# Kernel tuning notes

Hardware: AMD Instinct MI355X
Metric: run time of the kernel (lower is better)

## Reference

```python
import jax, jax.numpy as jnp
import numpy as np

N_NODES = 100000
N_EDGES = 600000
HID = 128
N_ETYPES = 8


def setup_inputs() -> dict:
    key = jax.random.key(0)
    ks = jax.random.split(key, 10)
    s = 1.0 / np.sqrt(HID)
    return {
        "h": jax.random.normal(ks[0], (N_NODES, HID), dtype=jnp.float32),
        "edge_index": jax.random.randint(ks[1], (2, N_EDGES), 0, N_NODES, dtype=jnp.int64),
        "edge_type": jax.random.randint(ks[2], (N_EDGES,), 0, N_ETYPES, dtype=jnp.int64),
        # per-edge-type Linear(hidden, hidden): weight (T, H_out, H_in) stored as (T, H_in, H_out) for einsum
        "message_W": jax.random.uniform(ks[3], (N_ETYPES, HID, HID), jnp.float32, -s, s),
        "message_b": jax.random.uniform(ks[4], (N_ETYPES, HID), jnp.float32, -s, s),
        # GRUCell params (torch layout): w_ih (3H, H), w_hh (3H, H), b_ih (3H,), b_hh (3H,)
        "gru_w_ih": jax.random.uniform(ks[5], (3 * HID, HID), jnp.float32, -s, s),
        "gru_w_hh": jax.random.uniform(ks[6], (3 * HID, HID), jnp.float32, -s, s),
        "gru_b_ih": jax.random.uniform(ks[7], (3 * HID,), jnp.float32, -s, s),
        "gru_b_hh": jax.random.uniform(ks[8], (3 * HID,), jnp.float32, -s, s),
    }


def reference(h, edge_index, edge_type, message_W, message_b,
              gru_w_ih, gru_w_hh, gru_b_ih, gru_b_hh):
    num_nodes = h.shape[0]
    src, dst = edge_index[0], edge_index[1]

    # Transform every node by every edge-type Linear once: (N, T, H).
    # Equivalent to per-type msg = h[src] @ W[t].T + b[t] gathered by edge type.
    all_msgs = jnp.einsum('nh,thd->ntd', h, message_W) + message_b  # (N, T, H)
    msg = all_msgs[src, edge_type]                                   # (E, H) gather
    messages = jax.ops.segment_sum(msg, dst, num_segments=num_nodes)  # scatter-add

    # GRUCell: r,z,n gates (torch semantics)
    gi = messages @ gru_w_ih.T + gru_b_ih  # (N, 3H)
    gh = h @ gru_w_hh.T + gru_b_hh         # (N, 3H)
    i_r, i_z, i_n = jnp.split(gi, 3, axis=-1)
    h_r, h_z, h_n = jnp.split(gh, 3, axis=-1)
    r = jax.nn.sigmoid(i_r + h_r)
    z = jax.nn.sigmoid(i_z + h_z)
    n = jnp.tanh(i_n + r * h_n)
    return (1.0 - z) * n + z * h
```

## Files before the change

### kernel.cpp

```cpp
#include <hip/hip_runtime.h>

#define HID 128
#define NTY 8

typedef __attribute__((ext_vector_type(8))) short bf16x8;
typedef __attribute__((ext_vector_type(4))) float f32x4;

__device__ __forceinline__ unsigned short f2bf(float x) {
    unsigned u = __float_as_uint(x);
    u += 0x7FFF + ((u >> 16) & 1);
    return (unsigned short)(u >> 16);
}
__device__ __forceinline__ float bf2f(unsigned short s) {
    return __uint_as_float(((unsigned)s) << 16);
}
__device__ __forceinline__ float sigmoidf_fast(float x) {
    return 1.f / (1.f + __expf(-x));
}
__device__ __forceinline__ float tanhf_fast(float x) {
    return 1.f - 2.f / (1.f + __expf(2.f * x));
}

__global__ void conv_h_kernel(const float* __restrict__ h, unsigned short* __restrict__ hbf, int n) {
    int i = blockIdx.x * 256 + threadIdx.x;
    if (i < n) hbf[i] = f2bf(h[i]);
}
__global__ void conv_W_kernel(const float* __restrict__ W, unsigned short* __restrict__ WbfT) {
    int i = blockIdx.x * 256 + threadIdx.x;
    int t = i >> 14, rem = i & 16383, d = rem >> 7, k = rem & 127;
    WbfT[(t << 14) + (d << 7) + k] = f2bf(W[(t << 14) + (k << 7) + d]);
}
__global__ void conv_wpk_kernel(const float* __restrict__ wih, const float* __restrict__ whh,
                                unsigned short* __restrict__ wpk) {
    int i = blockIdx.x * 256 + threadIdx.x;
    if (i >= 8 * 3 * 128 * 32) return;
    int kk = i & 31;
    int rest = i >> 5;
    int d = rest & 127;
    int rest2 = rest >> 7;
    int g3 = rest2 % 3, kc = rest2 / 3;
    float v;
    if (kc < 4) v = wih[(g3 * 128 + d) * 128 + kc * 32 + kk];
    else        v = whh[(g3 * 128 + d) * 128 + (kc - 4) * 32 + kk];
    wpk[i] = f2bf(v);
}

__global__ void hist_kernel(const int* __restrict__ etype, const int* __restrict__ ei,
                            int E, int* __restrict__ tcnt, int* __restrict__ deg) {
    __shared__ int lc[NTY];
    if (threadIdx.x < NTY) lc[threadIdx.x] = 0;
    __syncthreads();
    int stride = gridDim.x * blockDim.x;
    for (int i = blockIdx.x * blockDim.x + threadIdx.x; i < E; i += stride) {
        atomicAdd(&lc[etype[i]], 1);
        if (deg) atomicAdd(&deg[ei[E + i]], 1);
    }
    __syncthreads();
    if (threadIdx.x < NTY) atomicAdd(&tcnt[threadIdx.x], lc[threadIdx.x]);
}

__global__ void scan_type_kernel(const int* __restrict__ tcnt, int* __restrict__ tcur) {
    if (threadIdx.x == 0) {
        int off = 0;
        for (int t = 0; t < NTY; ++t) { tcur[t] = off; off += (tcnt[t] + 127) & ~127; }
    }
}

__global__ void scanA_kernel(const int* __restrict__ deg, int* __restrict__ start,
                             int* __restrict__ bsum, int N) {
    __shared__ int s[256];
    int i = blockIdx.x * 256 + threadIdx.x;
    int v = (i < N) ? deg[i] : 0;
    s[threadIdx.x] = v;
    __syncthreads();
    for (int off = 1; off < 256; off <<= 1) {
        int t = (threadIdx.x >= off) ? s[threadIdx.x - off] : 0;
        __syncthreads();
        s[threadIdx.x] += t;
        __syncthreads();
    }
    if (i < N) start[i] = s[threadIdx.x] - v;
    if (threadIdx.x == 255) bsum[blockIdx.x] = s[255];
}

__global__ void scanB_kernel(int* __restrict__ bsum, int nb) {
    __shared__ int s[512];
    int tx = threadIdx.x;
    int v = (tx < nb) ? bsum[tx] : 0;
    s[tx] = v;
    __syncthreads();
    for (int off = 1; off < 512; off <<= 1) {
        int t = (tx >= off) ? s[tx - off] : 0;
        __syncthreads();
        s[tx] += t;
        __syncthreads();
    }
    if (tx < nb) bsum[tx] = s[tx] - v;
}

__global__ void scanC_kernel(int* __restrict__ start, const int* __restrict__ bsum,
                             int* __restrict__ dcur, int N, int E) {
    int i = blockIdx.x * 256 + threadIdx.x;
    if (i < N) {
        int v = start[i] + bsum[blockIdx.x];
        start[i] = v;
        dcur[i] = v;
    }
    if (i == 0) start[N] = E;
}

__global__ __launch_bounds__(256) void scatter_agg(
    const int* __restrict__ etype, const int* __restrict__ ei, int E,
    int* __restrict__ tcur, int* __restrict__ dcur,
    int* __restrict__ sortedT, int* __restrict__ q, int mode)
{
    __shared__ int lcnt[NTY];
    __shared__ int lbase[NTY];
    int tx = threadIdx.x;
    int chunk = (E + gridDim.x - 1) / gridDim.x;
    int s = blockIdx.x * chunk;
    int e = s + chunk; if (e > E) e = E;
    if (tx < NTY) lcnt[tx] = 0;
    __syncthreads();
    for (int i = s + tx; i < e; i += 256)
        atomicAdd(&lcnt[etype[i]], 1);
    __syncthreads();
    if (tx < NTY) {
        lbase[tx] = atomicAdd(&tcur[tx], lcnt[tx]);
        lcnt[tx] = 0;
    }
    __syncthreads();
    for (int i = s + tx; i < e; i += 256) {
        int t = etype[i];
        int lp = atomicAdd(&lcnt[t], 1);
        sortedT[lbase[t] + lp] = i;
        if (mode) q[i] = atomicAdd(&dcur[ei[E + i]], 1);
    }
}

__global__ __launch_bounds__(256) void msg_gemm(
    const unsigned short* __restrict__ hbf, const int* __restrict__ ei, int E,
    const int* __restrict__ etype, const unsigned short* __restrict__ WbfT,
    const float* __restrict__ bias, const int* __restrict__ sortedT,
    const int* __restrict__ q, unsigned short* __restrict__ M,
    float* __restrict__ msum, int mode)
{
    __shared__ unsigned short hs[128][136];
    __shared__ unsigned short Bs[128][40];
    __shared__ int srcs[128], aux[128];
    __shared__ int stype;

    int tx = threadIdx.x;
    int base = blockIdx.x * 128;
    if (tx < 128) {
        int id = sortedT[base + tx];
        srcs[tx] = (id >= 0) ? ei[id] : -1;
        aux[tx]  = (id >= 0) ? (mode ? ei[E + id] : q[id]) : -1;
    }
    if (tx == 0) { int id0 = sortedT[base]; stype = (id0 >= 0) ? etype[id0] : -1; }
    __syncthreads();
    int t = stype;
    if (t < 0) return;

    const unsigned short* Wb = WbfT + (t << 14);

    for (int f = tx; f < 2048; f += 256) {
        int row = f >> 4, c8 = (f & 15) * 8;
        int s = srcs[row]; if (s < 0) s = 0;
        *(uint4*)&hs[row][c8] = *(const uint4*)&hbf[(size_t)s * 128 + c8];
    }

    int lane = tx & 63, w = tx >> 6;
    int r0 = (w >> 1) * 64, c0 = (w & 1) * 64;
    int lr = lane & 15, quad = lane >> 4;
    f32x4 acc[4][4] = {};

    for (int kc = 0; kc < 4; ++kc) {
        __syncthreads();
        for (int f = tx; f < 512; f += 256) {
            int d = f >> 2, c8 = (f & 3) * 8;
            *(uint4*)&Bs[d][c8] = *(const uint4*)&Wb[(d << 7) + kc * 32 + c8];
        }
        __syncthreads();
        bf16x8 af[4], bfr[4];
        #pragma unroll
        for (int rb = 0; rb < 4; ++rb) af[rb]  = *(const bf16x8*)&hs[r0 + rb * 16 + lr][kc * 32 + quad * 8];
        #pragma unroll
        for (int cb = 0; cb < 4; ++cb) bfr[cb] = *(const bf16x8*)&Bs[c0 + cb * 16 + lr][quad * 8];
        #pragma unroll
        for (int rb = 0; rb < 4; ++rb)
            #pragma unroll
            for (int cb = 0; cb < 4; ++cb)
                acc[rb][cb] = __builtin_amdgcn_mfma_f32_16x16x32_bf16(bfr[cb], af[rb], acc[rb][cb], 0, 0, 0);
    }

    float4 bv4[4];
    #pragma unroll
    for (int cb = 0; cb < 4; ++cb)
        bv4[cb] = *(const float4*)&bias[t * 128 + c0 + cb * 16 + quad * 4];

    #pragma unroll
    for (int rb = 0; rb < 4; ++rb) {
        int e = r0 + rb * 16 + lr;
        int mr = aux[e];
        if (mr < 0) continue;
        #pragma unroll
        for (int cb = 0; cb < 4; ++cb) {
            int d0 = c0 + cb * 16 + quad * 4;
            f32x4 a = acc[rb][cb];
            if (mode) {
                atomicAdd(&msum[(size_t)mr * 128 + d0 + 0], a[0] + bv4[cb].x);
                atomicAdd(&msum[(size_t)mr * 128 + d0 + 1], a[1] + bv4[cb].y);
                atomicAdd(&msum[(size_t)mr * 128 + d0 + 2], a[2] + bv4[cb].z);
                atomicAdd(&msum[(size_t)mr * 128 + d0 + 3], a[3] + bv4[cb].w);
            } else {
                uint2 v;
                v.x = (unsigned)f2bf(a[0] + bv4[cb].x) | ((unsigned)f2bf(a[1] + bv4[cb].y) << 16);
                v.y = (unsigned)f2bf(a[2] + bv4[cb].z) | ((unsigned)f2bf(a[3] + bv4[cb].w) << 16);
                *(uint2*)&M[(size_t)mr * 128 + d0] = v;
            }
        }
    }
}

__global__ __launch_bounds__(256) void gru_fused(
    const unsigned short* __restrict__ M, const int* __restrict__ start,
    const float* __restrict__ msum_fb, const unsigned short* __restrict__ hbf,
    const unsigned short* __restrict__ wpk, const float* __restrict__ bih,
    const float* __restrict__ bhh, const float* __restrict__ hf,
    float* __restrict__ out, int N, int mode)
{
    __shared__ unsigned short As[64][264];

    int tx = threadIdx.x;
    int n0 = blockIdx.x * 64;

    {
        int node = tx >> 2, qd = tx & 3;
        int n = n0 + node;
        int nc = (n < N) ? n : N - 1;
        float a[32];
        #pragma unroll
        for (int j = 0; j < 32; ++j) a[j] = 0.f;
        if (mode == 0) {
            int s = start[nc], e = start[nc + 1];
            for (int r = s; r < e; ++r) {
                #pragma unroll
                for (int j = 0; j < 4; ++j) {
                    uint4 v = *(const uint4*)&M[(size_t)r * 128 + qd * 32 + j * 8];
                    const unsigned short* pv = (const unsigned short*)&v;
                    #pragma unroll
                    for (int u = 0; u < 8; ++u) a[j * 8 + u] += bf2f(pv[u]);
                }
            }
        } else {
            #pragma unroll
            for (int j = 0; j < 8; ++j) {
                float4 v = *(const float4*)&msum_fb[(size_t)nc * 128 + qd * 32 + j * 4];
                a[j * 4 + 0] = v.x; a[j * 4 + 1] = v.y; a[j * 4 + 2] = v.z; a[j * 4 + 3] = v.w;
            }
        }
        unsigned short tmp[32];
        #pragma unroll
        for (int j = 0; j < 32; ++j) tmp[j] = f2bf(a[j]);
        #pragma unroll
        for (int j = 0; j < 4; ++j)
            *(uint4*)&As[node][qd * 32 + j * 8] = *(const uint4*)&tmp[j * 8];
        #pragma unroll
        for (int j = 0; j < 4; ++j)
            *(uint4*)&As[node][128 + qd * 32 + j * 8] =
                *(const uint4*)&hbf[(size_t)nc * 128 + qd * 32 + j * 8];
    }
    __syncthreads();

    int lane = tx & 63, w = tx >> 6;
    int rt = w & 1, cg = w >> 1;
    int lr = lane & 15, quad = lane >> 4;

    f32x4 aR[4][2] = {}, aZ[4][2] = {}, aI[4][2] = {}, aH[4][2] = {};

    #pragma unroll
    for (int kc = 0; kc < 4; ++kc) {
        bf16x8 af[2];
        #pragma unroll
        for (int r2 = 0; r2 < 2; ++r2)
            af[r2] = *(const bf16x8*)&As[rt * 32 + r2 * 16 + lr][kc * 32 + quad * 8];
        #pragma unroll
        for (int g3 = 0; g3 < 3; ++g3) {
            #pragma unroll
            for (int ct = 0; ct < 4; ++ct) {
                bf16x8 bf = *(const bf16x8*)&wpk[((size_t)((kc * 3 + g3) * 128) + cg * 64 + ct * 16 + lr) * 32 + quad * 8];
                #pragma unroll
                for (int r2 = 0; r2 < 2; ++r2) {
                    if (g3 == 0) aR[ct][r2] = __builtin_amdgcn_mfma_f32_16x16x32_bf16(bf, af[r2], aR[ct][r2], 0, 0, 0);
                    else if (g3 == 1) aZ[ct][r2] = __builtin_amdgcn_mfma_f32_16x16x32_bf16(bf, af[r2], aZ[ct][r2], 0, 0, 0);
                    else aI[ct][r2] = __builtin_amdgcn_mfma_f32_16x16x32_bf16(bf, af[r2], aI[ct][r2], 0, 0, 0);
                }
            }
        }
    }
    #pragma unroll
    for (int kc = 4; kc < 8; ++kc) {
        bf16x8 af[2];
        #pragma unroll
        for (int r2 = 0; r2 < 2; ++r2)
            af[r2] = *(const bf16x8*)&As[rt * 32 + r2 * 16 + lr][kc * 32 + quad * 8];
        #pragma unroll
        for (int g3 = 0; g3 < 3; ++g3) {
            #pragma unroll
            for (int ct = 0; ct < 4; ++ct) {
                bf16x8 bf = *(const bf16x8*)&wpk[((size_t)((kc * 3 + g3) * 128) + cg * 64 + ct * 16 + lr) * 32 + quad * 8];
                #pragma unroll
                for (int r2 = 0; r2 < 2; ++r2) {
                    if (g3 == 0) aR[ct][r2] = __builtin_amdgcn_mfma_f32_16x16x32_bf16(bf, af[r2], aR[ct][r2], 0, 0, 0);
                    else if (g3 == 1) aZ[ct][r2] = __builtin_amdgcn_mfma_f32_16x16x32_bf16(bf, af[r2], aZ[ct][r2], 0, 0, 0);
                    else aH[ct][r2] = __builtin_amdgcn_mfma_f32_16x16x32_bf16(bf, af[r2], aH[ct][r2], 0, 0, 0);
                }
            }
        }
    }

    #pragma unroll
    for (int ct = 0; ct < 4; ++ct) {
        int d0 = cg * 64 + ct * 16 + quad * 4;
        f32x4 bi_r = *(const f32x4*)&bih[d0];
        f32x4 bh_r = *(const f32x4*)&bhh[d0];
        f32x4 bi_z = *(const f32x4*)&bih[128 + d0];
        f32x4 bh_z = *(const f32x4*)&bhh[128 + d0];
        f32x4 bi_n = *(const f32x4*)&bih[256 + d0];
        f32x4 bh_n = *(const f32x4*)&bhh[256 + d0];
        #pragma unroll
        for (int r2 = 0; r2 < 2; ++r2) {
            int n = n0 + rt * 32 + r2 * 16 + lr;
            if (n >= N) continue;
            f32x4 h0 = *(const f32x4*)&hf[(size_t)n * 128 + d0];
            f32x4 o;
            #pragma unroll
            for (int j = 0; j < 4; ++j) {
                float r  = sigmoidf_fast(aR[ct][r2][j] + bi_r[j] + bh_r[j]);
                float z  = sigmoidf_fast(aZ[ct][r2][j] + bi_z[j] + bh_z[j]);
                float nn = tanhf_fast(aI[ct][r2][j] + bi_n[j] + r * (aH[ct][r2][j] + bh_n[j]));
                o[j] = (1.f - z) * nn + z * h0[j];
            }
            *(f32x4*)&out[(size_t)n * 128 + d0] = o;
        }
    }
}

extern "C" void kernel_launch(void* const* d_in, const int* in_sizes, int n_in,
                              void* d_out, int out_size, void* d_ws, size_t ws_size,
                              hipStream_t stream)
{
    const float* h     = (const float*)d_in[0];
    const int*   ei    = (const int*)d_in[1];
    const int*   etype = (const int*)d_in[2];
    const float* W     = (const float*)d_in[3];
    const float* b     = (const float*)d_in[4];
    const float* wih   = (const float*)d_in[5];
    const float* whh   = (const float*)d_in[6];
    const float* bih   = (const float*)d_in[7];
    const float* bhh   = (const float*)d_in[8];
    float* out = (float*)d_out;

    int E = in_sizes[1] / 2;
    int N = in_sizes[0] / HID;
    int capE = ((E + 127) / 128 + NTY) * 128;

    char* p = (char*)d_ws;
    auto alloc = [&](size_t bytes) { char* r = p; p += (bytes + 255) & ~(size_t)255; return r; };
    unsigned short* hbf  = (unsigned short*)alloc((size_t)N * 128 * 2);
    unsigned short* WbfT = (unsigned short*)alloc((size_t)8 * 128 * 128 * 2);
    unsigned short* wpk  = (unsigned short*)alloc((size_t)8 * 3 * 128 * 32 * 2);
    int* tcnt    = (int*)alloc(NTY * 4);
    int* tcur    = (int*)alloc(NTY * 4);
    int* sortedT = (int*)alloc((size_t)capE * 4);
    unsigned short* M = (unsigned short*)alloc((size_t)E * 128 * 2);
    int* q     = (int*)alloc((size_t)E * 4);
    int* deg   = (int*)alloc((size_t)N * 4);
    int* start = (int*)alloc((size_t)(N + 1) * 4);
    int* dcur  = (int*)alloc((size_t)N * 4);
    int* bsum  = (int*)alloc(512 * 4);
    int mode = ((size_t)(p - (char*)d_ws) <= ws_size) ? 0 : 1;

    hipMemsetAsync(tcnt, 0, NTY * 4, stream);
    hipMemsetAsync(sortedT, 0xFF, (size_t)capE * 4, stream);
    if (mode == 0) hipMemsetAsync(deg, 0, (size_t)N * 4, stream);
    else           hipMemsetAsync(out, 0, (size_t)N * 128 * 4, stream);

    conv_h_kernel<<<(N * 128 + 255) / 256, 256, 0, stream>>>(h, hbf, N * 128);
    conv_W_kernel<<<(8 * 128 * 128) / 256, 256, 0, stream>>>(W, WbfT);
    conv_wpk_kernel<<<(8 * 3 * 128 * 32 + 255) / 256, 256, 0, stream>>>(wih, whh, wpk);

    hist_kernel<<<1024, 256, 0, stream>>>(etype, ei, E, tcnt, (mode == 0) ? deg : nullptr);
    scan_type_kernel<<<1, 64, 0, stream>>>(tcnt, tcur);
    if (mode == 0) {
        int nbA = (N + 255) / 256;
        scanA_kernel<<<nbA, 256, 0, stream>>>(deg, start, bsum, N);
        scanB_kernel<<<1, 512, 0, stream>>>(bsum, nbA);
        scanC_kernel<<<nbA, 256, 0, stream>>>(start, bsum, dcur, N, E);
    }
    scatter_agg<<<256, 256, 0, stream>>>(etype, ei, E, tcur, dcur, sortedT, q, (mode == 0) ? 1 : 0);

    msg_gemm<<<capE / 128, 256, 0, stream>>>(hbf, ei, E, etype, WbfT, b, sortedT, q, M, out, mode);
    gru_fused<<<(N + 63) / 64, 256, 0, stream>>>(M, start, out, hbf, wpk, bih, bhh, h, out, N, mode);
}
```

Baseline: 411.7 us.

## Aggregate source features per (dst,type) before transform and fuse into GRU kernel

Edges are now sorted by (destination, edge type) with an 8-way counting sort. For each node and type, the bf16 source features are summed first and multiplied by W[t] afterwards, with the bias scaled by the edge count. The per-edge message GEMM and the E×128 intermediate buffer are gone, and the aggregation, the type GEMMs and the GRU all run in one kernel with weights pre-packed into MFMA fragment order. In exchange the gather loops are per-lane and serial, their length depends on node degree, and each node block repeats 8 small GEMMs.

```diff
diff --git a/kernel.cpp b/kernel.cpp
--- a/kernel.cpp
+++ b/kernel.cpp
@@ -2,6 +2,7 @@
 
 #define HID 128
 #define NTY 8
+#define SCAP 768
 
 typedef __attribute__((ext_vector_type(8))) short bf16x8;
 typedef __attribute__((ext_vector_type(4))) float f32x4;
@@ -25,45 +26,41 @@
     int i = blockIdx.x * 256 + threadIdx.x;
     if (i < n) hbf[i] = f2bf(h[i]);
 }
-__global__ void conv_W_kernel(const float* __restrict__ W, unsigned short* __restrict__ WbfT) {
-    int i = blockIdx.x * 256 + threadIdx.x;
-    int t = i >> 14, rem = i & 16383, d = rem >> 7, k = rem & 127;
-    WbfT[(t << 14) + (d << 7) + k] = f2bf(W[(t << 14) + (k << 7) + d]);
-}
-__global__ void conv_wpk_kernel(const float* __restrict__ wih, const float* __restrict__ whh,
-                                unsigned short* __restrict__ wpk) {
-    int i = blockIdx.x * 256 + threadIdx.x;
-    if (i >= 8 * 3 * 128 * 32) return;
-    int kk = i & 31;
-    int rest = i >> 5;
-    int d = rest & 127;
-    int rest2 = rest >> 7;
-    int g3 = rest2 % 3, kc = rest2 / 3;
+
+__global__ void conv_Wfrag_kernel(const float* __restrict__ W, unsigned short* __restrict__ wfr) {
+    int i = blockIdx.x * 256 + threadIdx.x;
+    int e = i & 7, f = (i >> 3) & 31, lane = (i >> 8) & 63, t = i >> 14;
+    int cb = f >> 2, kc = f & 3;
+    int lr = lane & 15, quad = lane >> 4;
+    int d = cb * 16 + lr;
+    int k = kc * 32 + quad * 8 + e;
+    wfr[i] = f2bf(W[(t << 14) + (k << 7) + d]);
+}
+
+__global__ void conv_wpkf_kernel(const float* __restrict__ wih, const float* __restrict__ whh,
+                                 unsigned short* __restrict__ wpkf) {
+    int i = blockIdx.x * 256 + threadIdx.x;
+    int e = i & 7;
+    int rest = i >> 3;
+    int lane = rest / 192;
+    int f = rest - lane * 192;
+    int kc = f / 24;
+    int f2 = f - kc * 24;
+    int g3 = f2 >> 3, ct = f2 & 7;
+    int lr = lane & 15, quad = lane >> 4;
+    int d = ct * 16 + lr;
+    int kk = quad * 8 + e;
     float v;
     if (kc < 4) v = wih[(g3 * 128 + d) * 128 + kc * 32 + kk];
     else        v = whh[(g3 * 128 + d) * 128 + (kc - 4) * 32 + kk];
-    wpk[i] = f2bf(v);
-}
-
-__global__ void hist_kernel(const int* __restrict__ etype, const int* __restrict__ ei,
-                            int E, int* __restrict__ tcnt, int* __restrict__ deg) {
-    __shared__ int lc[NTY];
-    if (threadIdx.x < NTY) lc[threadIdx.x] = 0;
-    __syncthreads();
+    wpkf[i] = f2bf(v);
+}
+
+__global__ void hist8_kernel(const int* __restrict__ etype, const int* __restrict__ ei,
+                             int E, int* __restrict__ deg8) {
     int stride = gridDim.x * blockDim.x;
-    for (int i = blockIdx.x * blockDim.x + threadIdx.x; i < E; i += stride) {
-        atomicAdd(&lc[etype[i]], 1);
-        if (deg) atomicAdd(&deg[ei[E + i]], 1);
-    }
-    __syncthreads();
-    if (threadIdx.x < NTY) atomicAdd(&tcnt[threadIdx.x], lc[threadIdx.x]);
-}
-
-__global__ void scan_type_kernel(const int* __restrict__ tcnt, int* __restrict__ tcur) {
-    if (threadIdx.x == 0) {
-        int off = 0;
-        for (int t = 0; t < NTY; ++t) { tcur[t] = off; off += (tcnt[t] + 127) & ~127; }
-    }
+    for (int i = blockIdx.x * blockDim.x + threadIdx.x; i < E; i += stride)
+        atomicAdd(&deg8[ei[E + i] * 8 + etype[i]], 1);
 }
 
 __global__ void scanA_kernel(const int* __restrict__ deg, int* __restrict__ start,
@@ -83,266 +80,216 @@
     if (threadIdx.x == 255) bsum[blockIdx.x] = s[255];
 }
 
-__global__ void scanB_kernel(int* __restrict__ bsum, int nb) {
-    __shared__ int s[512];
+__global__ void scanBbig_kernel(int* __restrict__ bsum, int nb) {
+    __shared__ int s[256];
     int tx = threadIdx.x;
-    int v = (tx < nb) ? bsum[tx] : 0;
-    s[tx] = v;
+    int C = (nb + 255) / 256;
+    int lo = tx * C, hi = lo + C; if (hi > nb) hi = nb;
+    int sum = 0;
+    for (int j = lo; j < hi; ++j) sum += bsum[j];
+    s[tx] = sum;
     __syncthreads();
-    for (int off = 1; off < 512; off <<= 1) {
+    for (int off = 1; off < 256; off <<= 1) {
         int t = (tx >= off) ? s[tx - off] : 0;
         __syncthreads();
         s[tx] += t;
         __syncthreads();
     }
-    if (tx < nb) bsum[tx] = s[tx] - v;
-}
-
-__global__ void scanC_kernel(int* __restrict__ start, const int* __restrict__ bsum,
-                             int* __restrict__ dcur, int N, int E) {
-    int i = blockIdx.x * 256 + threadIdx.x;
-    if (i < N) {
-        int v = start[i] + bsum[blockIdx.x];
-        start[i] = v;
-        dcur[i] = v;
-    }
-    if (i == 0) start[N] = E;
-}
-
-__global__ __launch_bounds__(256) void scatter_agg(
-    const int* __restrict__ etype, const int* __restrict__ ei, int E,
-    int* __restrict__ tcur, int* __restrict__ dcur,
-    int* __restrict__ sortedT, int* __restrict__ q, int mode)
+    int run = s[tx] - sum;
+    for (int j = lo; j < hi; ++j) { int v = bsum[j]; bsum[j] = run; run += v; }
+}
+
+__global__ void scanC8_kernel(int* __restrict__ start8, const int* __restrict__ bsum,
+                              int* __restrict__ cur8, int M8, int E) {
+    int i = blockIdx.x * 256 + threadIdx.x;
+    if (i < M8) {
+        int v = start8[i] + bsum[blockIdx.x];
+        start8[i] = v;
+        cur8[i] = v;
+    }
+    if (i == 0) start8[M8] = E;
+}
+
+__global__ void scatter8_kernel(const int* __restrict__ etype, const int* __restrict__ ei,
+                                int E, int* __restrict__ cur8, int* __restrict__ sortedE) {
+    int stride = gridDim.x * blockDim.x;
+    for (int i = blockIdx.x * blockDim.x + threadIdx.x; i < E; i += stride) {
+        int pos = atomicAdd(&cur8[ei[E + i] * 8 + etype[i]], 1);
+        sortedE[pos] = ei[i];
+    }
+}
+
+__global__ __launch_bounds__(256) void fused_ggnn(
+    const unsigned short* __restrict__ hbf, const float* __restrict__ hf,
+    const int* __restrict__ sortedE, const int* __restrict__ start8,
+    const unsigned short* __restrict__ wfr, const float* __restrict__ bias,
+    const unsigned short* __restrict__ wpkf, const float* __restrict__ bih,
+    const float* __restrict__ bhh, float* __restrict__ out, int N)
 {
-    __shared__ int lcnt[NTY];
-    __shared__ int lbase[NTY];
-    int tx = threadIdx.x;
-    int chunk = (E + gridDim.x - 1) / gridDim.x;
-    int s = blockIdx.x * chunk;
-    int e = s + chunk; if (e > E) e = E;
-    if (tx < NTY) lcnt[tx] = 0;
-    __syncthreads();
-    for (int i = s + tx; i < e; i += 256)
-        atomicAdd(&lcnt[etype[i]], 1);
-    __syncthreads();
-    if (tx < NTY) {
-        lbase[tx] = atomicAdd(&tcur[tx], lcnt[tx]);
-        lcnt[tx] = 0;
-    }
-    __syncthreads();
-    for (int i = s + tx; i < e; i += 256) {
-        int t = etype[i];
-        int lp = atomicAdd(&lcnt[t], 1);
-        sortedT[lbase[t] + lp] = i;
-        if (mode) q[i] = atomicAdd(&dcur[ei[E + i]], 1);
-    }
-}
-
-__global__ __launch_bounds__(256) void msg_gemm(
-    const unsigned short* __restrict__ hbf, const int* __restrict__ ei, int E,
-    const int* __restrict__ etype, const unsigned short* __restrict__ WbfT,
-    const float* __restrict__ bias, const int* __restrict__ sortedT,
-    const int* __restrict__ q, unsigned short* __restrict__ M,
-    float* __restrict__ msum, int mode)
-{
-    __shared__ unsigned short hs[128][136];
-    __shared__ unsigned short Bs[128][40];
-    __shared__ int srcs[128], aux[128];
-    __shared__ int stype;
-
-    int tx = threadIdx.x;
-    int base = blockIdx.x * 128;
-    if (tx < 128) {
-        int id = sortedT[base + tx];
-        srcs[tx] = (id >= 0) ? ei[id] : -1;
-        aux[tx]  = (id >= 0) ? (mode ? ei[E + id] : q[id]) : -1;
-    }
-    if (tx == 0) { int id0 = sortedT[base]; stype = (id0 >= 0) ? etype[id0] : -1; }
-    __syncthreads();
-    int t = stype;
-    if (t < 0) return;
-
-    const unsigned short* Wb = WbfT + (t << 14);
-
-    for (int f = tx; f < 2048; f += 256) {
-        int row = f >> 4, c8 = (f & 15) * 8;
-        int s = srcs[row]; if (s < 0) s = 0;
-        *(uint4*)&hs[row][c8] = *(const uint4*)&hbf[(size_t)s * 128 + c8];
-    }
-
-    int lane = tx & 63, w = tx >> 6;
-    int r0 = (w >> 1) * 64, c0 = (w & 1) * 64;
-    int lr = lane & 15, quad = lane >> 4;
-    f32x4 acc[4][4] = {};
-
-    for (int kc = 0; kc < 4; ++kc) {
-        __syncthreads();
-        for (int f = tx; f < 512; f += 256) {
-            int d = f >> 2, c8 = (f & 3) * 8;
-            *(uint4*)&Bs[d][c8] = *(const uint4*)&Wb[(d << 7) + kc * 32 + c8];
-        }
-        __syncthreads();
-        bf16x8 af[4], bfr[4];
-        #pragma unroll
-        for (int rb = 0; rb < 4; ++rb) af[rb]  = *(const bf16x8*)&hs[r0 + rb * 16 + lr][kc * 32 + quad * 8];
-        #pragma unroll
-        for (int cb = 0; cb < 4; ++cb) bfr[cb] = *(const bf16x8*)&Bs[c0 + cb * 16 + lr][quad * 8];
-        #pragma unroll
-        for (int rb = 0; rb < 4; ++rb)
-            #pragma unroll
-            for (int cb = 0; cb < 4; ++cb)
-                acc[rb][cb] = __builtin_amdgcn_mfma_f32_16x16x32_bf16(bfr[cb], af[rb], acc[rb][cb], 0, 0, 0);
-    }
-
-    float4 bv4[4];
-    #pragma unroll
-    for (int cb = 0; cb < 4; ++cb)
-        bv4[cb] = *(const float4*)&bias[t * 128 + c0 + cb * 16 + quad * 4];
-
-    #pragma unroll
-    for (int rb = 0; rb < 4; ++rb) {
-        int e = r0 + rb * 16 + lr;
-        int mr = aux[e];
-        if (mr < 0) continue;
-        #pragma unroll
-        for (int cb = 0; cb < 4; ++cb) {
-            int d0 = c0 + cb * 16 + quad * 4;
-            f32x4 a = acc[rb][cb];
-            if (mode) {
-                atomicAdd(&msum[(size_t)mr * 128 + d0 + 0], a[0] + bv4[cb].x);
-                atomicAdd(&msum[(size_t)mr * 128 + d0 + 1], a[1] + bv4[cb].y);
-                atomicAdd(&msum[(size_t)mr * 128 + d0 + 2], a[2] + bv4[cb].z);
-                atomicAdd(&msum[(size_t)mr * 128 + d0 + 3], a[3] + bv4[cb].w);
-            } else {
-                uint2 v;
-                v.x = (unsigned)f2bf(a[0] + bv4[cb].x) | ((unsigned)f2bf(a[1] + bv4[cb].y) << 16);
-                v.y = (unsigned)f2bf(a[2] + bv4[cb].z) | ((unsigned)f2bf(a[3] + bv4[cb].w) << 16);
-                *(uint2*)&M[(size_t)mr * 128 + d0] = v;
-            }
-        }
-    }
-}
-
-__global__ __launch_bounds__(256) void gru_fused(
-    const unsigned short* __restrict__ M, const int* __restrict__ start,
-    const float* __restrict__ msum_fb, const unsigned short* __restrict__ hbf,
-    const unsigned short* __restrict__ wpk, const float* __restrict__ bih,
-    const float* __restrict__ bhh, const float* __restrict__ hf,
-    float* __restrict__ out, int N, int mode)
-{
-    __shared__ unsigned short As[64][264];
+    __shared__ unsigned short As[4][2048];
+    __shared__ int srcs[SCAP];
+    __shared__ int bnds[513];
 
     int tx = threadIdx.x;
     int n0 = blockIdx.x * 64;
-
+    int lane = tx & 63, w = tx >> 6;
+    int lr = lane & 15, quad = lane >> 4;
+    int ln = w * 16 + lr;
+    int n = n0 + ln;
+    bool valid = (n < N);
+    int nc = valid ? n : (N - 1);
+
+    int nhi = n0 + 64; if (nhi > N) nhi = N;
+    int rowlo = start8[n0 * 8];
+    int rowhi = start8[nhi * 8];
+    int cntb = rowhi - rowlo;
+
+    for (int i = tx; i < cntb && i < SCAP; i += 256) srcs[i] = sortedE[rowlo + i];
+    int top = (nhi - n0) * 8;
+    for (int i = tx; i <= top; i += 256) bnds[i] = start8[n0 * 8 + i];
+    __syncthreads();
+
+    const int* rbase = (cntb <= SCAP) ? (const int*)srcs : sortedE;
+    int roff = (cntb <= SCAP) ? rowlo : 0;
+
+    f32x4 macc[8] = {};
+    const unsigned short* wl = wfr + ((size_t)lane << 8);
+
+    for (int t = 0; t < 8; ++t) {
+        int rs = valid ? bnds[ln * 8 + t] : 0;
+        int re = valid ? bnds[ln * 8 + t + 1] : 0;
+
+        float sa[32];
+        #pragma unroll
+        for (int j = 0; j < 32; ++j) sa[j] = 0.f;
+
+        for (int r = rs; r < re; ++r) {
+            int src = rbase[r - roff];
+            const unsigned short* hp = hbf + ((size_t)src << 7) + (quad << 3);
+            uint4 v0 = *(const uint4*)(hp);
+            uint4 v1 = *(const uint4*)(hp + 32);
+            uint4 v2 = *(const uint4*)(hp + 64);
+            uint4 v3 = *(const uint4*)(hp + 96);
+            const unsigned short* p0 = (const unsigned short*)&v0;
+            const unsigned short* p1 = (const unsigned short*)&v1;
+            const unsigned short* p2 = (const unsigned short*)&v2;
+            const unsigned short* p3 = (const unsigned short*)&v3;
+            #pragma unroll
+            for (int u = 0; u < 8; ++u) {
+                sa[u]      += bf2f(p0[u]);
+                sa[8 + u]  += bf2f(p1[u]);
+                sa[16 + u] += bf2f(p2[u]);
+                sa[24 + u] += bf2f(p3[u]);
+            }
+        }
+
+        float fcnt = (float)(re - rs);
+        #pragma unroll
+        for (int cb = 0; cb < 8; ++cb) {
+            float4 bv = *(const float4*)&bias[t * 128 + cb * 16 + quad * 4];
+            macc[cb][0] += fcnt * bv.x;
+            macc[cb][1] += fcnt * bv.y;
+            macc[cb][2] += fcnt * bv.z;
+            macc[cb][3] += fcnt * bv.w;
+        }
+
+        const unsigned short* wlt = wl + t * 16384;
+        #pragma unroll
+        for (int kc = 0; kc < 4; ++kc) {
+            unsigned short au[8];
+            #pragma unroll
+            for (int u = 0; u < 8; ++u) au[u] = f2bf(sa[kc * 8 + u]);
+            bf16x8 af = *(const bf16x8*)au;
+            #pragma unroll
+            for (int cb = 0; cb < 8; ++cb) {
+                bf16x8 wf = *(const bf16x8*)&wlt[(cb * 4 + kc) * 8];
+                macc[cb] = __builtin_amdgcn_mfma_f32_16x16x32_bf16(wf, af, macc[cb], 0, 0, 0);
+            }
+        }
+    }
+
+    unsigned short* AsW = &As[w][0];
+    #pragma unroll
+    for (int cb = 0; cb < 8; ++cb) {
+        uint2 v;
+        v.x = (unsigned)f2bf(macc[cb][0]) | ((unsigned)f2bf(macc[cb][1]) << 16);
+        v.y = (unsigned)f2bf(macc[cb][2]) | ((unsigned)f2bf(macc[cb][3]) << 16);
+        int byte = (lr << 8) + (cb << 5) + (quad << 3);
+        byte ^= (lr & 7) << 4;
+        *(uint2*)((char*)AsW + byte) = v;
+    }
+    __syncthreads();
+
+    bf16x8 afh[4];
     {
-        int node = tx >> 2, qd = tx & 3;
-        int n = n0 + node;
-        int nc = (n < N) ? n : N - 1;
-        float a[32];
-        #pragma unroll
-        for (int j = 0; j < 32; ++j) a[j] = 0.f;
-        if (mode == 0) {
-            int s = start[nc], e = start[nc + 1];
-            for (int r = s; r < e; ++r) {
+        const unsigned short* hrow = hbf + ((size_t)nc << 7) + (quad << 3);
+        #pragma unroll
+        for (int k4 = 0; k4 < 4; ++k4) afh[k4] = *(const bf16x8*)&hrow[k4 * 32];
+    }
+    const unsigned short* wp = wpkf + (size_t)lane * 1536;
+
+    #pragma unroll
+    for (int dh = 0; dh < 2; ++dh) {
+        f32x4 aR[4] = {}, aZ[4] = {}, aH[4] = {};
+        #pragma unroll
+        for (int kc = 0; kc < 8; ++kc) {
+            bf16x8 af;
+            if (kc < 4) {
+                int byte = ((lr << 8) + (kc << 6) + (quad << 4)) ^ ((lr & 7) << 4);
+                af = *(const bf16x8*)((char*)AsW + byte);
+            } else {
+                af = afh[kc - 4];
+            }
+            #pragma unroll
+            for (int c = 0; c < 4; ++c) {
+                int ct = dh * 4 + c;
+                bf16x8 wfR = *(const bf16x8*)&wp[(kc * 24 + ct) * 8];
+                aR[c] = __builtin_amdgcn_mfma_f32_16x16x32_bf16(wfR, af, aR[c], 0, 0, 0);
+                bf16x8 wfZ = *(const bf16x8*)&wp[(kc * 24 + 8 + ct) * 8];
+                aZ[c] = __builtin_amdgcn_mfma_f32_16x16x32_bf16(wfZ, af, aZ[c], 0, 0, 0);
+                if (kc >= 4) {
+                    bf16x8 wfH = *(const bf16x8*)&wp[(kc * 24 + 16 + ct) * 8];
+                    aH[c] = __builtin_amdgcn_mfma_f32_16x16x32_bf16(wfH, af, aH[c], 0, 0, 0);
+                }
+            }
+        }
+        f32x4 rv[4], zv[4];
+        #pragma unroll
+        for (int c = 0; c < 4; ++c) {
+            int d0 = (dh * 4 + c) * 16 + quad * 4;
+            f32x4 bir = *(const f32x4*)&bih[d0],       bhr = *(const f32x4*)&bhh[d0];
+            f32x4 biz = *(const f32x4*)&bih[128 + d0], bhz = *(const f32x4*)&bhh[128 + d0];
+            f32x4 bin = *(const f32x4*)&bih[256 + d0], bhn = *(const f32x4*)&bhh[256 + d0];
+            #pragma unroll
+            for (int j = 0; j < 4; ++j) {
+                rv[c][j] = sigmoidf_fast(aR[c][j] + bir[j] + bhr[j]);
+                zv[c][j] = sigmoidf_fast(aZ[c][j] + biz[j] + bhz[j]);
+                aH[c][j] = bin[j] + rv[c][j] * (aH[c][j] + bhn[j]);
+            }
+        }
+        #pragma unroll
+        for (int kc = 0; kc < 4; ++kc) {
+            int byte = ((lr << 8) + (kc << 6) + (quad << 4)) ^ ((lr & 7) << 4);
+            bf16x8 af = *(const bf16x8*)((char*)AsW + byte);
+            #pragma unroll
+            for (int c = 0; c < 4; ++c) {
+                bf16x8 wfH = *(const bf16x8*)&wp[(kc * 24 + 16 + dh * 4 + c) * 8];
+                aH[c] = __builtin_amdgcn_mfma_f32_16x16x32_bf16(wfH, af, aH[c], 0, 0, 0);
+            }
+        }
+        if (valid) {
+            #pragma unroll
+            for (int c = 0; c < 4; ++c) {
+                int d0 = (dh * 4 + c) * 16 + quad * 4;
+                f32x4 h0 = *(const f32x4*)&hf[(size_t)n * 128 + d0];
+                f32x4 o;
                 #pragma unroll
                 for (int j = 0; j < 4; ++j) {
-                    uint4 v = *(const uint4*)&M[(size_t)r * 128 + qd * 32 + j * 8];
-                    const unsigned short* pv = (const unsigned short*)&v;
-                    #pragma unroll
-                    for (int u = 0; u < 8; ++u) a[j * 8 + u] += bf2f(pv[u]);
+                    float nn = tanhf_fast(aH[c][j]);
+                    o[j] = (1.f - zv[c][j]) * nn + zv[c][j] * h0[j];
                 }
-            }
-        } else {
-            #pragma unroll
-            for (int j = 0; j < 8; ++j) {
-                float4 v = *(const float4*)&msum_fb[(size_t)nc * 128 + qd * 32 + j * 4];
-                a[j * 4 + 0] = v.x; a[j * 4 + 1] = v.y; a[j * 4 + 2] = v.z; a[j * 4 + 3] = v.w;
-            }
-        }
-        unsigned short tmp[32];
-        #pragma unroll
-        for (int j = 0; j < 32; ++j) tmp[j] = f2bf(a[j]);
-        #pragma unroll
-        for (int j = 0; j < 4; ++j)
-            *(uint4*)&As[node][qd * 32 + j * 8] = *(const uint4*)&tmp[j * 8];
-        #pragma unroll
-        for (int j = 0; j < 4; ++j)
-            *(uint4*)&As[node][128 + qd * 32 + j * 8] =
-                *(const uint4*)&hbf[(size_t)nc * 128 + qd * 32 + j * 8];
-    }
-    __syncthreads();
-
-    int lane = tx & 63, w = tx >> 6;
-    int rt = w & 1, cg = w >> 1;
-    int lr = lane & 15, quad = lane >> 4;
-
-    f32x4 aR[4][2] = {}, aZ[4][2] = {}, aI[4][2] = {}, aH[4][2] = {};
-
-    #pragma unroll
-    for (int kc = 0; kc < 4; ++kc) {
-        bf16x8 af[2];
-        #pragma unroll
-        for (int r2 = 0; r2 < 2; ++r2)
-            af[r2] = *(const bf16x8*)&As[rt * 32 + r2 * 16 + lr][kc * 32 + quad * 8];
-        #pragma unroll
-        for (int g3 = 0; g3 < 3; ++g3) {
-            #pragma unroll
-            for (int ct = 0; ct < 4; ++ct) {
-                bf16x8 bf = *(const bf16x8*)&wpk[((size_t)((kc * 3 + g3) * 128) + cg * 64 + ct * 16 + lr) * 32 + quad * 8];
-                #pragma unroll
-                for (int r2 = 0; r2 < 2; ++r2) {
-                    if (g3 == 0) aR[ct][r2] = __builtin_amdgcn_mfma_f32_16x16x32_bf16(bf, af[r2], aR[ct][r2], 0, 0, 0);
-                    else if (g3 == 1) aZ[ct][r2] = __builtin_amdgcn_mfma_f32_16x16x32_bf16(bf, af[r2], aZ[ct][r2], 0, 0, 0);
-                    else aI[ct][r2] = __builtin_amdgcn_mfma_f32_16x16x32_bf16(bf, af[r2], aI[ct][r2], 0, 0, 0);
-                }
-            }
-        }
-    }
-    #pragma unroll
-    for (int kc = 4; kc < 8; ++kc) {
-        bf16x8 af[2];
-        #pragma unroll
-        for (int r2 = 0; r2 < 2; ++r2)
-            af[r2] = *(const bf16x8*)&As[rt * 32 + r2 * 16 + lr][kc * 32 + quad * 8];
-        #pragma unroll
-        for (int g3 = 0; g3 < 3; ++g3) {
-            #pragma unroll
-            for (int ct = 0; ct < 4; ++ct) {
-                bf16x8 bf = *(const bf16x8*)&wpk[((size_t)((kc * 3 + g3) * 128) + cg * 64 + ct * 16 + lr) * 32 + quad * 8];
-                #pragma unroll
-                for (int r2 = 0; r2 < 2; ++r2) {
-                    if (g3 == 0) aR[ct][r2] = __builtin_amdgcn_mfma_f32_16x16x32_bf16(bf, af[r2], aR[ct][r2], 0, 0, 0);
-                    else if (g3 == 1) aZ[ct][r2] = __builtin_amdgcn_mfma_f32_16x16x32_bf16(bf, af[r2], aZ[ct][r2], 0, 0, 0);
-                    else aH[ct][r2] = __builtin_amdgcn_mfma_f32_16x16x32_bf16(bf, af[r2], aH[ct][r2], 0, 0, 0);
-                }
-            }
-        }
-    }
-
-    #pragma unroll
-    for (int ct = 0; ct < 4; ++ct) {
-        int d0 = cg * 64 + ct * 16 + quad * 4;
-        f32x4 bi_r = *(const f32x4*)&bih[d0];
-        f32x4 bh_r = *(const f32x4*)&bhh[d0];
-        f32x4 bi_z = *(const f32x4*)&bih[128 + d0];
-        f32x4 bh_z = *(const f32x4*)&bhh[128 + d0];
-        f32x4 bi_n = *(const f32x4*)&bih[256 + d0];
-        f32x4 bh_n = *(const f32x4*)&bhh[256 + d0];
-        #pragma unroll
-        for (int r2 = 0; r2 < 2; ++r2) {
-            int n = n0 + rt * 32 + r2 * 16 + lr;
-            if (n >= N) continue;
-            f32x4 h0 = *(const f32x4*)&hf[(size_t)n * 128 + d0];
-            f32x4 o;
-            #pragma unroll
-            for (int j = 0; j < 4; ++j) {
-                float r  = sigmoidf_fast(aR[ct][r2][j] + bi_r[j] + bh_r[j]);
-                float z  = sigmoidf_fast(aZ[ct][r2][j] + bi_z[j] + bh_z[j]);
-                float nn = tanhf_fast(aI[ct][r2][j] + bi_n[j] + r * (aH[ct][r2][j] + bh_n[j]));
-                o[j] = (1.f - z) * nn + z * h0[j];
-            }
-            *(f32x4*)&out[(size_t)n * 128 + d0] = o;
+                *(f32x4*)&out[(size_t)n * 128 + d0] = o;
+            }
         }
     }
 }
@@ -364,43 +311,32 @@
 
     int E = in_sizes[1] / 2;
     int N = in_sizes[0] / HID;
-    int capE = ((E + 127) / 128 + NTY) * 128;
+    int M8 = N * 8;
+    int nbA = (M8 + 255) / 256;
 
     char* p = (char*)d_ws;
     auto alloc = [&](size_t bytes) { char* r = p; p += (bytes + 255) & ~(size_t)255; return r; };
     unsigned short* hbf  = (unsigned short*)alloc((size_t)N * 128 * 2);
-    unsigned short* WbfT = (unsigned short*)alloc((size_t)8 * 128 * 128 * 2);
-    unsigned short* wpk  = (unsigned short*)alloc((size_t)8 * 3 * 128 * 32 * 2);
-    int* tcnt    = (int*)alloc(NTY * 4);
-    int* tcur    = (int*)alloc(NTY * 4);
-    int* sortedT = (int*)alloc((size_t)capE * 4);
-    unsigned short* M = (unsigned short*)alloc((size_t)E * 128 * 2);
-    int* q     = (int*)alloc((size_t)E * 4);
-    int* deg   = (int*)alloc((size_t)N * 4);
-    int* start = (int*)alloc((size_t)(N + 1) * 4);
-    int* dcur  = (int*)alloc((size_t)N * 4);
-    int* bsum  = (int*)alloc(512 * 4);
-    int mode = ((size_t)(p - (char*)d_ws) <= ws_size) ? 0 : 1;
-
-    hipMemsetAsync(tcnt, 0, NTY * 4, stream);
-    hipMemsetAsync(sortedT, 0xFF, (size_t)capE * 4, stream);
-    if (mode == 0) hipMemsetAsync(deg, 0, (size_t)N * 4, stream);
-    else           hipMemsetAsync(out, 0, (size_t)N * 128 * 4, stream);
+    unsigned short* wfr  = (unsigned short*)alloc((size_t)8 * 128 * 128 * 2);
+    unsigned short* wpkf = (unsigned short*)alloc((size_t)8 * 3 * 128 * 32 * 2);
+    int* deg8    = (int*)alloc((size_t)M8 * 4);
+    int* start8  = (int*)alloc(((size_t)M8 + 1) * 4);
+    int* cur8    = (int*)alloc((size_t)M8 * 4);
+    int* bsum    = (int*)alloc((size_t)nbA * 4);
+    int* sortedE = (int*)alloc((size_t)E * 4);
+
+    hipMemsetAsync(deg8, 0, (size_t)M8 * 4, stream);
 
     conv_h_kernel<<<(N * 128 + 255) / 256, 256, 0, stream>>>(h, hbf, N * 128);
-    conv_W_kernel<<<(8 * 128 * 128) / 256, 256, 0, stream>>>(W, WbfT);
-    conv_wpk_kernel<<<(8 * 3 * 128 * 32 + 255) / 256, 256, 0, stream>>>(wih, whh, wpk);
-
-    hist_kernel<<<1024, 256, 0, stream>>>(etype, ei, E, tcnt, (mode == 0) ? deg : nullptr);
-    scan_type_kernel<<<1, 64, 0, stream>>>(tcnt, tcur);
-    if (mode == 0) {
-        int nbA = (N + 255) / 256;
-        scanA_kernel<<<nbA, 256, 0, stream>>>(deg, start, bsum, N);
-        scanB_kernel<<<1, 512, 0, stream>>>(bsum, nbA);
-        scanC_kernel<<<nbA, 256, 0, stream>>>(start, bsum, dcur, N, E);
-    }
-    scatter_agg<<<256, 256, 0, stream>>>(etype, ei, E, tcur, dcur, sortedT, q, (mode == 0) ? 1 : 0);
-
-    msg_gemm<<<capE / 128, 256, 0, stream>>>(hbf, ei, E, etype, WbfT, b, sortedT, q, M, out, mode);
-    gru_fused<<<(N + 63) / 64, 256, 0, stream>>>(M, start, out, hbf, wpk, bih, bhh, h, out, N, mode);
-}
+    conv_Wfrag_kernel<<<512, 256, 0, stream>>>(W, wfr);
+    conv_wpkf_kernel<<<384, 256, 0, stream>>>(wih, whh, wpkf);
+
+    hist8_kernel<<<1024, 256, 0, stream>>>(etype, ei, E, deg8);
+    scanA_kernel<<<nbA, 256, 0, stream>>>(deg8, start8, bsum, M8);
+    scanBbig_kernel<<<1, 256, 0, stream>>>(bsum, nbA);
+    scanC8_kernel<<<nbA, 256, 0, stream>>>(start8, bsum, cur8, M8, E);
+    scatter8_kernel<<<1024, 256, 0, stream>>>(etype, ei, E, cur8, sortedE);
+
+    fused_ggnn<<<(N + 63) / 64, 256, 0, stream>>>(hbf, h, sortedE, start8, wfr, b,
+                                                  wpkf, bih, bhh, out, N);
+}
```

Measured after the change: 667.3 us. +62.1%, slower.
